# Performance work log

Measured on AMD Instinct MI355X. Metric: run time of the kernel, lower is better.

## Reference

```python
import jax, jax.numpy as jnp
import numpy as np

B, N, D, H, DEG = 2, 20000, 256, 8, 8
E = N * DEG
EPS = 1e-3  # keras LayerNormalization default epsilon


def layer_norm(x, gamma, beta):
    mu = jnp.mean(x, axis=-1, keepdims=True)
    var = jnp.mean(jnp.square(x - mu), axis=-1, keepdims=True)
    return (x - mu) * jax.lax.rsqrt(var + EPS) * gamma + beta


def setup_inputs() -> dict:
    key = jax.random.key(0)
    ks = jax.random.split(key, 8)
    x = jax.random.normal(ks[0], (B, N, D), dtype=jnp.float32)
    # edge list sorted by source node; every node has DEG out-edges so
    # segment_sum covers all N segments (matches tf.math.segment_sum semantics)
    src = jnp.repeat(jnp.arange(N, dtype=jnp.int64), DEG)
    dst = jax.random.randint(ks[1], (E,), 0, N, dtype=jnp.int64)
    edges = jnp.stack([src, dst], axis=1)  # [E, 2]
    scale = 0.05
    wq = jax.random.normal(ks[2], (D, D), dtype=jnp.float32) * scale
    wk = jax.random.normal(ks[3], (D, D), dtype=jnp.float32) * scale
    wv = jax.random.normal(ks[4], (D, D), dtype=jnp.float32) * scale
    wo = jax.random.normal(ks[5], (D, D), dtype=jnp.float32) * scale
    zeros = jnp.zeros((D,), dtype=jnp.float32)
    ones = jnp.ones((D,), dtype=jnp.float32)
    return {
        "x": x, "edges": edges,
        "wq": wq, "bq": zeros, "wk": wk, "bk": zeros,
        "wv": wv, "bv": zeros, "wo": wo, "bo": zeros,
        "gamma1": ones, "beta1": zeros, "gamma2": ones, "beta2": zeros,
    }


def reference(x, edges, wq, bq, wk, bk, wv, bv, wo, bo, gamma1, beta1, gamma2, beta2):
    b, n, d = x.shape
    h, dh = H, D // H
    xn = layer_norm(x, gamma1, beta1)                      # [B,N,D]
    # QKV projections, split heads, move node axis to front: [N,B,H,dh]
    def proj(w, bias):
        y = (xn @ w + bias).reshape(b, n, h, dh)
        return jnp.transpose(y, (1, 0, 2, 3))
    q, k, v = proj(wq, bq), proj(wk, bk), proj(wv, bv)
    src, dst = edges[:, 0], edges[:, 1]
    q_part = q[src]                                         # [E,B,H,dh]
    k_part = k[dst]
    v_part = v[dst]
    logits = jnp.sum(q_part * k_part, axis=-1, keepdims=True) / jnp.sqrt(
        jnp.asarray(dh, dtype=x.dtype))                     # [E,B,H,1]
    w = jnp.exp(logits)                                     # unnormalized softmax (as in source)
    num = jax.ops.segment_sum(v_part * w, src, num_segments=n)  # [N,B,H,dh]
    den = jax.ops.segment_sum(w, src, num_segments=n)           # [N,B,H,1]
    attn = num / den
    attn = jnp.transpose(attn, (1, 0, 2, 3)).reshape(b, n, d)   # [B,N,D]
    concat = xn + attn                                      # residual uses normed input (source reassigns `inputs`)
    out = layer_norm(concat, gamma2, beta2)
    out = jax.nn.relu(out @ wo + bo)
    return out + concat
```

## Files before the change

### kernel.cpp

```cpp
#include <hip/hip_runtime.h>


typedef __bf16 bf16x8 __attribute__((ext_vector_type(8)));
typedef float  f32x4  __attribute__((ext_vector_type(4)));

__device__ __forceinline__ float bf2f(unsigned short u) {
    union { unsigned int i; float f; } v; v.i = ((unsigned int)u) << 16; return v.f;
}
__device__ __forceinline__ unsigned short f2bf(float f) {
    union { float f; unsigned int i; } v; v.f = f;
    unsigned int x = v.i;
    unsigned int r = (x + 0x7FFFu + ((x >> 16) & 1u)) >> 16;
    return (unsigned short)r;
}

#define NNODE 20000
#define ROWS  40000
#define DMODEL 256

__global__ __launch_bounds__(256) void prep_ln1_kernel(
    const float* __restrict__ wq, const float* __restrict__ wk,
    const float* __restrict__ wv, const float* __restrict__ wo,
    const float* __restrict__ bq, const float* __restrict__ bk,
    const float* __restrict__ bv, const float* __restrict__ bo,
    const float* __restrict__ x,
    const float* __restrict__ g1, const float* __restrict__ b1,
    unsigned short* __restrict__ Wqkvt,
    unsigned short* __restrict__ Wot,
    float* __restrict__ biasq,
    float* __restrict__ biaso,
    unsigned short* __restrict__ xn)
{
    if (blockIdx.x < 1024) {
        int idx = blockIdx.x * 256 + threadIdx.x;
        if (idx < 768 * 256) {
            int n = idx >> 8, k = idx & 255;
            int sel = n >> 8, nl = n & 255;
            const float* w = (sel == 0) ? wq : (sel == 1) ? wk : wv;
            Wqkvt[idx] = f2bf(w[k * 256 + nl]);
        } else {
            int idx2 = idx - 768 * 256;
            int n = idx2 >> 8, k = idx2 & 255;
            Wot[idx2] = f2bf(wo[k * 256 + n]);
        }
        if (idx < 768) {
            const float* bb = (idx < 256) ? bq : (idx < 512) ? bk : bv;
            biasq[idx] = bb[idx & 255];
        }
        if (idx >= 768 && idx < 1024) biaso[idx - 768] = bo[idx - 768];
        return;
    }
    int wave = threadIdx.x >> 6, lane = threadIdx.x & 63;
    int sub = lane >> 5, hl = lane & 31;
    int m = (blockIdx.x - 1024) * 8 + wave * 2 + sub;
    const float* xp = x + (size_t)m * DMODEL + hl * 8;
    float4 x0 = *(const float4*)xp;
    float4 x1 = *(const float4*)(xp + 4);
    float f[8] = {x0.x, x0.y, x0.z, x0.w, x1.x, x1.y, x1.z, x1.w};
    float s = 0.f, ss = 0.f;
    #pragma unroll
    for (int t = 0; t < 8; ++t) { s += f[t]; ss += f[t]*f[t]; }
    #pragma unroll
    for (int mk = 1; mk < 32; mk <<= 1) { s += __shfl_xor(s, mk); ss += __shfl_xor(ss, mk); }
    float mu  = s * (1.f/256.f);
    float var = ss * (1.f/256.f) - mu*mu;
    float rs  = rsqrtf(var + 1e-3f);
    float4 g0 = *(const float4*)(g1 + hl * 8);
    float4 g1v = *(const float4*)(g1 + hl * 8 + 4);
    float4 b0 = *(const float4*)(b1 + hl * 8);
    float4 b1v = *(const float4*)(b1 + hl * 8 + 4);
    float gg[8] = {g0.x, g0.y, g0.z, g0.w, g1v.x, g1v.y, g1v.z, g1v.w};
    float bb[8] = {b0.x, b0.y, b0.z, b0.w, b1v.x, b1v.y, b1v.z, b1v.w};
    unsigned short o[8];
    #pragma unroll
    for (int t = 0; t < 8; ++t) o[t] = f2bf((f[t] - mu) * rs * gg[t] + bb[t]);
    *(int4*)(xn + (size_t)m * DMODEL + hl * 8) = *(const int4*)o;
}

#define LDS_W 72
#define MFMA_BF16(d, a, b) d = __builtin_amdgcn_mfma_f32_16x16x32_bf16(a, b, d, 0, 0, 0)

template<bool EPI>
__global__ __launch_bounds__(256, 2) void gemm_kernel(
    const unsigned short* __restrict__ A,
    const unsigned short* __restrict__ Bt,
    const float* __restrict__ bias,
    void* __restrict__ C,
    const unsigned short* __restrict__ resid,
    int M, int Ncols)
{
    __shared__ unsigned short As[128 * LDS_W];
    __shared__ unsigned short Bs[128 * LDS_W];
    int tid  = threadIdx.x;
    int wave = tid >> 6, lane = tid & 63;
    int quad = lane >> 4, l16 = lane & 15;

    int nt_total = Ncols >> 7;
    int nwg = gridDim.x;
    int xcd = blockIdx.x & 7, loc = blockIdx.x >> 3;
    int qq = nwg >> 3, rr = nwg & 7;
    int wid = (xcd < rr) ? (xcd * (qq + 1) + loc)
                         : (rr * (qq + 1) + (xcd - rr) * qq + loc);
    int mt = wid / nt_total;
    int nt = wid - mt * nt_total;
    int m0 = mt * 128, n0 = nt * 128;
    int wm = (wave >> 1) * 64, wn = (wave & 1) * 64;

    int srow = tid >> 1;
    int sseg = (tid & 1) * 32;
    int arow = m0 + srow; if (arow >= M) arow = M - 1;
    const unsigned short* ArowP = A  + (size_t)arow * 256 + sseg;
    const unsigned short* BrowP = Bt + (size_t)(n0 + srow) * 256 + sseg;
    unsigned short* AsP = &As[srow * LDS_W + sseg];
    unsigned short* BsP = &Bs[srow * LDS_W + sseg];

    f32x4 acc00 = {}, acc01 = {}, acc02 = {}, acc03 = {};
    f32x4 acc10 = {}, acc11 = {}, acc12 = {}, acc13 = {};
    f32x4 acc20 = {}, acc21 = {}, acc22 = {}, acc23 = {};
    f32x4 acc30 = {}, acc31 = {}, acc32 = {}, acc33 = {};

    int4 va0 = *(const int4*)(ArowP);
    int4 va1 = *(const int4*)(ArowP + 8);
    int4 va2 = *(const int4*)(ArowP + 16);
    int4 va3 = *(const int4*)(ArowP + 24);
    int4 vb0 = *(const int4*)(BrowP);
    int4 vb1 = *(const int4*)(BrowP + 8);
    int4 vb2 = *(const int4*)(BrowP + 16);
    int4 vb3 = *(const int4*)(BrowP + 24);

    for (int kt = 0; kt < 4; ++kt) {
        __syncthreads();
        *(int4*)(AsP)      = va0;
        *(int4*)(AsP + 8)  = va1;
        *(int4*)(AsP + 16) = va2;
        *(int4*)(AsP + 24) = va3;
        *(int4*)(BsP)      = vb0;
        *(int4*)(BsP + 8)  = vb1;
        *(int4*)(BsP + 16) = vb2;
        *(int4*)(BsP + 24) = vb3;
        __syncthreads();
        if (kt < 3) {
            const unsigned short* ap = ArowP + (kt + 1) * 64;
            const unsigned short* bp = BrowP + (kt + 1) * 64;
            va0 = *(const int4*)(ap);
            va1 = *(const int4*)(ap + 8);
            va2 = *(const int4*)(ap + 16);
            va3 = *(const int4*)(ap + 24);
            vb0 = *(const int4*)(bp);
            vb1 = *(const int4*)(bp + 8);
            vb2 = *(const int4*)(bp + 16);
            vb3 = *(const int4*)(bp + 24);
        }
        #pragma unroll
        for (int ks = 0; ks < 64; ks += 32) {
            bf16x8 a0 = *(const bf16x8*)&As[(wm +  0 + l16) * LDS_W + ks + quad * 8];
            bf16x8 a1 = *(const bf16x8*)&As[(wm + 16 + l16) * LDS_W + ks + quad * 8];
            bf16x8 a2 = *(const bf16x8*)&As[(wm + 32 + l16) * LDS_W + ks + quad * 8];
            bf16x8 a3 = *(const bf16x8*)&As[(wm + 48 + l16) * LDS_W + ks + quad * 8];
            bf16x8 b0 = *(const bf16x8*)&Bs[(wn +  0 + l16) * LDS_W + ks + quad * 8];
            bf16x8 b1 = *(const bf16x8*)&Bs[(wn + 16 + l16) * LDS_W + ks + quad * 8];
            bf16x8 b2 = *(const bf16x8*)&Bs[(wn + 32 + l16) * LDS_W + ks + quad * 8];
            bf16x8 b3 = *(const bf16x8*)&Bs[(wn + 48 + l16) * LDS_W + ks + quad * 8];
            MFMA_BF16(acc00, a0, b0); MFMA_BF16(acc01, a0, b1);
            MFMA_BF16(acc02, a0, b2); MFMA_BF16(acc03, a0, b3);
            MFMA_BF16(acc10, a1, b0); MFMA_BF16(acc11, a1, b1);
            MFMA_BF16(acc12, a1, b2); MFMA_BF16(acc13, a1, b3);
            MFMA_BF16(acc20, a2, b0); MFMA_BF16(acc21, a2, b1);
            MFMA_BF16(acc22, a2, b2); MFMA_BF16(acc23, a2, b3);
            MFMA_BF16(acc30, a3, b0); MFMA_BF16(acc31, a3, b1);
            MFMA_BF16(acc32, a3, b2); MFMA_BF16(acc33, a3, b3);
        }
    }

#define EPI_STORE(accv, R, CC) do {                                          \
        int col = n0 + wn + (CC) * 16 + l16;                                 \
        float bb = bias[col];                                                \
        int rowb = m0 + wm + (R) * 16 + quad * 4;                            \
        _Pragma("unroll")                                                    \
        for (int rr = 0; rr < 4; ++rr) {                                     \
            int row = rowb + rr;                                             \
            if (row < M) {                                                   \
                float v = (accv)[rr] + bb;                                   \
                if (EPI) {                                                   \
                    v = fmaxf(v, 0.f);                                       \
                    v += bf2f(resid[(size_t)row * 256 + col]);               \
                    ((float*)C)[(size_t)row * Ncols + col] = v;              \
                } else {                                                     \
                    ((unsigned short*)C)[(size_t)row * Ncols + col] = f2bf(v);\
                }                                                            \
            }                                                                \
        }                                                                    \
    } while (0)

    EPI_STORE(acc00, 0, 0); EPI_STORE(acc01, 0, 1); EPI_STORE(acc02, 0, 2); EPI_STORE(acc03, 0, 3);
    EPI_STORE(acc10, 1, 0); EPI_STORE(acc11, 1, 1); EPI_STORE(acc12, 1, 2); EPI_STORE(acc13, 1, 3);
    EPI_STORE(acc20, 2, 0); EPI_STORE(acc21, 2, 1); EPI_STORE(acc22, 2, 2); EPI_STORE(acc23, 2, 3);
    EPI_STORE(acc30, 3, 0); EPI_STORE(acc31, 3, 1); EPI_STORE(acc32, 3, 2); EPI_STORE(acc33, 3, 3);
#undef EPI_STORE
}

__global__ __launch_bounds__(1024) void attn_kernel(
    const unsigned short* __restrict__ qkv,
    const int* __restrict__ edges,
    const unsigned short* __restrict__ xn,
    const float* __restrict__ g2, const float* __restrict__ b2,
    unsigned short* __restrict__ concat,
    unsigned short* __restrict__ h2,
    int node0)
{
    int wave = threadIdx.x >> 6, lane = threadIdx.x & 63;
    int i = node0 + blockIdx.x * 16 + wave;
    int b = lane >> 5, hl = lane & 31;
    size_t m = (size_t)b * NNODE + i;

    int jv = 0;
    if (lane < 8) jv = edges[2 * (i * 8 + lane) + 1];

    int4 qi = *(const int4*)(qkv + m * 768 + hl * 8);
    int4 xi = *(const int4*)(xn + m * DMODEL + hl * 8);
    const unsigned short* qs = (const unsigned short*)&qi;
    float qf[8];
    #pragma unroll
    for (int t = 0; t < 8; ++t) qf[t] = bf2f(qs[t]);

#define KVLOAD(E)                                                                  \
    int j##E = __shfl(jv, E);                                                      \
    const unsigned short* kp##E = qkv + ((size_t)b * NNODE + j##E) * 768 + 256 + hl * 8; \
    int4 KI##E = *(const int4*)(kp##E);                                            \
    int4 VI##E = *(const int4*)(kp##E + 256);
    KVLOAD(0) KVLOAD(1) KVLOAD(2) KVLOAD(3)
    KVLOAD(4) KVLOAD(5) KVLOAD(6) KVLOAD(7)
#undef KVLOAD

    float acc[8] = {};
    float den = 0.f;
    const float scale = 0.17677669529663687f;
#define EDGE(E) do {                                                         \
        const unsigned short* ks = (const unsigned short*)&KI##E;            \
        const unsigned short* vs = (const unsigned short*)&VI##E;            \
        float dot = 0.f;                                                     \
        _Pragma("unroll")                                                    \
        for (int t = 0; t < 8; ++t) dot += qf[t] * bf2f(ks[t]);              \
        dot += __shfl_xor(dot, 1);                                           \
        dot += __shfl_xor(dot, 2);               \
        float w = __expf(dot * scale);                                       \
        _Pragma("unroll")                                                    \
        for (int t = 0; t < 8; ++t) acc[t] += w * bf2f(vs[t]);               \
        den += w;                                                            \
    } while (0)
    EDGE(0); EDGE(1); EDGE(2); EDGE(3);
    EDGE(4); EDGE(5); EDGE(6); EDGE(7);
#undef EDGE
    float inv = 1.f / den;

    const unsigned short* xs = (const unsigned short*)&xi;
    float c[8], s = 0.f, ss = 0.f;
    #pragma unroll
    for (int t = 0; t < 8; ++t) { c[t] = bf2f(xs[t]) + acc[t] * inv; s += c[t]; ss += c[t]*c[t]; }
    #pragma unroll
    for (int mk = 1; mk < 32; mk <<= 1) { s += __shfl_xor(s, mk); ss += __shfl_xor(ss, mk); }
    float mu  = s * (1.f/256.f);
    float var = ss * (1.f/256.f) - mu*mu;
    float rs  = rsqrtf(var + 1e-3f);

    float4 ga = *(const float4*)(g2 + hl * 8);
    float4 gb = *(const float4*)(g2 + hl * 8 + 4);
    float4 ba = *(const float4*)(b2 + hl * 8);
    float4 bb = *(const float4*)(b2 + hl * 8 + 4);
    float gg[8] = {ga.x, ga.y, ga.z, ga.w, gb.x, gb.y, gb.z, gb.w};
    float bv[8] = {ba.x, ba.y, ba.z, ba.w, bb.x, bb.y, bb.z, bb.w};
    unsigned short oc[8], oh[8];
    #pragma unroll
    for (int t = 0; t < 8; ++t) {
        oc[t] = f2bf(c[t]);
        oh[t] = f2bf((c[t] - mu) * rs * gg[t] + bv[t]);
    }
    *(int4*)(concat + m * DMODEL + hl * 8) = *(const int4*)oc;
    *(int4*)(h2     + m * DMODEL + hl * 8) = *(const int4*)oh;
}

extern "C" void kernel_launch(void* const* d_in, const int* in_sizes, int n_in,
                              void* d_out, int out_size, void* d_ws, size_t ws_size,
                              hipStream_t stream)
{
    const float* x   = (const float*)d_in[0];
    const int* edges = (const int*)d_in[1];
    const float* wq = (const float*)d_in[2];
    const float* bq = (const float*)d_in[3];
    const float* wk = (const float*)d_in[4];
    const float* bk = (const float*)d_in[5];
    const float* wv = (const float*)d_in[6];
    const float* bv = (const float*)d_in[7];
    const float* wo = (const float*)d_in[8];
    const float* bo = (const float*)d_in[9];
    const float* g1 = (const float*)d_in[10];
    const float* b1 = (const float*)d_in[11];
    const float* g2 = (const float*)d_in[12];
    const float* b2 = (const float*)d_in[13];

    char* ws = (char*)d_ws;
    unsigned short* Wqkvt = (unsigned short*)(ws);
    unsigned short* Wot   = (unsigned short*)(ws + 393216);
    float* biasq          = (float*)(ws + 393216 + 131072);
    float* biaso          = (float*)(ws + 393216 + 131072 + 3072);
    size_t off = 393216 + 131072 + 4096;
    unsigned short* xn     = (unsigned short*)(ws + off); off += (size_t)ROWS * DMODEL * 2;
    unsigned short* qkv    = (unsigned short*)(ws + off); off += (size_t)ROWS * 768 * 2;
    unsigned short* concat = (unsigned short*)(ws + off); off += (size_t)ROWS * DMODEL * 2;
    unsigned short* h2     = (unsigned short*)(ws + off); off += (size_t)ROWS * DMODEL * 2;

    prep_ln1_kernel<<<1024 + ROWS / 8, 256, 0, stream>>>(
        wq, wk, wv, wo, bq, bk, bv, bo, x, g1, b1, Wqkvt, Wot, biasq, biaso, xn);
    gemm_kernel<false><<<dim3(313 * 6), 256, 0, stream>>>(xn, Wqkvt, biasq, qkv, nullptr, ROWS, 768);
    attn_kernel<<<625, 1024, 0, stream>>>(qkv, edges, xn, g2, b2, concat, h2, 0);
    attn_kernel<<<625, 1024, 0, stream>>>(qkv, edges, xn, g2, b2, concat, h2, 10000);
    gemm_kernel<true><<<dim3(313 * 2), 256, 0, stream>>>(h2, Wot, biaso, d_out, concat, ROWS, 256);
}
```

Baseline: 232.6 us.

## Load GEMM MFMA operands directly from global memory, drop LDS staging

```diff
diff --git a/kernel.cpp b/kernel.cpp
--- a/kernel.cpp
+++ b/kernel.cpp
@@ -77,7 +77,6 @@
     *(int4*)(xn + (size_t)m * DMODEL + hl * 8) = *(const int4*)o;
 }
 
-#define LDS_W 72
 #define MFMA_BF16(d, a, b) d = __builtin_amdgcn_mfma_f32_16x16x32_bf16(a, b, d, 0, 0, 0)
 
 template<bool EPI>
@@ -89,8 +88,6 @@
     const unsigned short* __restrict__ resid,
     int M, int Ncols)
 {
-    __shared__ unsigned short As[128 * LDS_W];
-    __shared__ unsigned short Bs[128 * LDS_W];
     int tid  = threadIdx.x;
     int wave = tid >> 6, lane = tid & 63;
     int quad = lane >> 4, l16 = lane & 15;
@@ -106,70 +103,43 @@
     int m0 = mt * 128, n0 = nt * 128;
     int wm = (wave >> 1) * 64, wn = (wave & 1) * 64;
 
-    int srow = tid >> 1;
-    int sseg = (tid & 1) * 32;
-    int arow = m0 + srow; if (arow >= M) arow = M - 1;
-    const unsigned short* ArowP = A  + (size_t)arow * 256 + sseg;
-    const unsigned short* BrowP = Bt + (size_t)(n0 + srow) * 256 + sseg;
-    unsigned short* AsP = &As[srow * LDS_W + sseg];
-    unsigned short* BsP = &Bs[srow * LDS_W + sseg];
+    int ar0 = m0 + wm +  0 + l16; if (ar0 >= M) ar0 = M - 1;
+    int ar1 = m0 + wm + 16 + l16; if (ar1 >= M) ar1 = M - 1;
+    int ar2 = m0 + wm + 32 + l16; if (ar2 >= M) ar2 = M - 1;
+    int ar3 = m0 + wm + 48 + l16; if (ar3 >= M) ar3 = M - 1;
+    const unsigned short* pa0 = A + (size_t)ar0 * 256 + quad * 8;
+    const unsigned short* pa1 = A + (size_t)ar1 * 256 + quad * 8;
+    const unsigned short* pa2 = A + (size_t)ar2 * 256 + quad * 8;
+    const unsigned short* pa3 = A + (size_t)ar3 * 256 + quad * 8;
+    const unsigned short* pb0 = Bt + (size_t)(n0 + wn +  0 + l16) * 256 + quad * 8;
+    const unsigned short* pb1 = Bt + (size_t)(n0 + wn + 16 + l16) * 256 + quad * 8;
+    const unsigned short* pb2 = Bt + (size_t)(n0 + wn + 32 + l16) * 256 + quad * 8;
+    const unsigned short* pb3 = Bt + (size_t)(n0 + wn + 48 + l16) * 256 + quad * 8;
 
     f32x4 acc00 = {}, acc01 = {}, acc02 = {}, acc03 = {};
     f32x4 acc10 = {}, acc11 = {}, acc12 = {}, acc13 = {};
     f32x4 acc20 = {}, acc21 = {}, acc22 = {}, acc23 = {};
     f32x4 acc30 = {}, acc31 = {}, acc32 = {}, acc33 = {};
 
-    int4 va0 = *(const int4*)(ArowP);
-    int4 va1 = *(const int4*)(ArowP + 8);
-    int4 va2 = *(const int4*)(ArowP + 16);
-    int4 va3 = *(const int4*)(ArowP + 24);
-    int4 vb0 = *(const int4*)(BrowP);
-    int4 vb1 = *(const int4*)(BrowP + 8);
-    int4 vb2 = *(const int4*)(BrowP + 16);
-    int4 vb3 = *(const int4*)(BrowP + 24);
-
-    for (int kt = 0; kt < 4; ++kt) {
-        __syncthreads();
-        *(int4*)(AsP)      = va0;
-        *(int4*)(AsP + 8)  = va1;
-        *(int4*)(AsP + 16) = va2;
-        *(int4*)(AsP + 24) = va3;
-        *(int4*)(BsP)      = vb0;
-        *(int4*)(BsP + 8)  = vb1;
-        *(int4*)(BsP + 16) = vb2;
-        *(int4*)(BsP + 24) = vb3;
-        __syncthreads();
-        if (kt < 3) {
-            const unsigned short* ap = ArowP + (kt + 1) * 64;
-            const unsigned short* bp = BrowP + (kt + 1) * 64;
-            va0 = *(const int4*)(ap);
-            va1 = *(const int4*)(ap + 8);
-            va2 = *(const int4*)(ap + 16);
-            va3 = *(const int4*)(ap + 24);
-            vb0 = *(const int4*)(bp);
-            vb1 = *(const int4*)(bp + 8);
-            vb2 = *(const int4*)(bp + 16);
-            vb3 = *(const int4*)(bp + 24);
-        }
-        #pragma unroll
-        for (int ks = 0; ks < 64; ks += 32) {
-            bf16x8 a0 = *(const bf16x8*)&As[(wm +  0 + l16) * LDS_W + ks + quad * 8];
-            bf16x8 a1 = *(const bf16x8*)&As[(wm + 16 + l16) * LDS_W + ks + quad * 8];
-            bf16x8 a2 = *(const bf16x8*)&As[(wm + 32 + l16) * LDS_W + ks + quad * 8];
-            bf16x8 a3 = *(const bf16x8*)&As[(wm + 48 + l16) * LDS_W + ks + quad * 8];
-            bf16x8 b0 = *(const bf16x8*)&Bs[(wn +  0 + l16) * LDS_W + ks + quad * 8];
-            bf16x8 b1 = *(const bf16x8*)&Bs[(wn + 16 + l16) * LDS_W + ks + quad * 8];
-            bf16x8 b2 = *(const bf16x8*)&Bs[(wn + 32 + l16) * LDS_W + ks + quad * 8];
-            bf16x8 b3 = *(const bf16x8*)&Bs[(wn + 48 + l16) * LDS_W + ks + quad * 8];
-            MFMA_BF16(acc00, a0, b0); MFMA_BF16(acc01, a0, b1);
-            MFMA_BF16(acc02, a0, b2); MFMA_BF16(acc03, a0, b3);
-            MFMA_BF16(acc10, a1, b0); MFMA_BF16(acc11, a1, b1);
-            MFMA_BF16(acc12, a1, b2); MFMA_BF16(acc13, a1, b3);
-            MFMA_BF16(acc20, a2, b0); MFMA_BF16(acc21, a2, b1);
-            MFMA_BF16(acc22, a2, b2); MFMA_BF16(acc23, a2, b3);
-            MFMA_BF16(acc30, a3, b0); MFMA_BF16(acc31, a3, b1);
-            MFMA_BF16(acc32, a3, b2); MFMA_BF16(acc33, a3, b3);
-        }
+    #pragma unroll
+    for (int kk = 0; kk < 8; ++kk) {
+        int off = kk * 32;
+        bf16x8 a0 = *(const bf16x8*)(pa0 + off);
+        bf16x8 a1 = *(const bf16x8*)(pa1 + off);
+        bf16x8 a2 = *(const bf16x8*)(pa2 + off);
+        bf16x8 a3 = *(const bf16x8*)(pa3 + off);
+        bf16x8 b0 = *(const bf16x8*)(pb0 + off);
+        bf16x8 b1 = *(const bf16x8*)(pb1 + off);
+        bf16x8 b2 = *(const bf16x8*)(pb2 + off);
+        bf16x8 b3 = *(const bf16x8*)(pb3 + off);
+        MFMA_BF16(acc00, a0, b0); MFMA_BF16(acc01, a0, b1);
+        MFMA_BF16(acc02, a0, b2); MFMA_BF16(acc03, a0, b3);
+        MFMA_BF16(acc10, a1, b0); MFMA_BF16(acc11, a1, b1);
+        MFMA_BF16(acc12, a1, b2); MFMA_BF16(acc13, a1, b3);
+        MFMA_BF16(acc20, a2, b0); MFMA_BF16(acc21, a2, b1);
+        MFMA_BF16(acc22, a2, b2); MFMA_BF16(acc23, a2, b3);
+        MFMA_BF16(acc30, a3, b0); MFMA_BF16(acc31, a3, b1);
+        MFMA_BF16(acc32, a3, b2); MFMA_BF16(acc33, a3, b3);
     }
 
 #define EPI_STORE(accv, R, CC) do {                                          \
```

Result: slower. 299.7 us (+28.9%).
